# Optimization experiments

Hardware: AMD Instinct MI355X
Metric: run time of the kernel (lower is better)

## Reference

```python
import jax, jax.numpy as jnp
import numpy as np

N_NODES = 20000
IN_DIM = 128      # in_dim(125) + 3
HIDDEN = 256
HEADS = 3
OUT_DIM = 384
NEG_SLOPE = 0.2


def _glorot(key, shape):
    fan_in, fan_out = shape[0], shape[-1]
    lim = (6.0 / (fan_in + fan_out)) ** 0.5
    return jax.random.uniform(key, shape, jnp.float32, -lim, lim)


def setup_inputs() -> dict:
    key = jax.random.key(0)
    ks = jax.random.split(key, 12)
    x = jax.random.normal(ks[0], (N_NODES, IN_DIM), jnp.float32)
    edge_index = jax.random.randint(ks[1], (2, 320000), 0, N_NODES, jnp.int64)
    return {
        "x": x,
        "edge_index": edge_index,
        # gat1: IN_DIM -> HEADS*HIDDEN (concat)
        "W1": _glorot(ks[2], (IN_DIM, HEADS * HIDDEN)),
        "att_src1": _glorot(ks[3], (HEADS, HIDDEN)),
        "att_dst1": _glorot(ks[4], (HEADS, HIDDEN)),
        "b1": jnp.zeros((HEADS * HIDDEN,), jnp.float32),
        # gat2: HEADS*HIDDEN -> OUT_DIM (1 head)
        "W2": _glorot(ks[5], (HEADS * HIDDEN, OUT_DIM)),
        "att_src2": _glorot(ks[6], (1, OUT_DIM)),
        "att_dst2": _glorot(ks[7], (1, OUT_DIM)),
        "b2": jnp.zeros((OUT_DIM,), jnp.float32),
    }


def _gat_layer(x, src, dst, W, a_src, a_dst, bias, heads, out_ch):
    """PyG GATConv: per-head linear, LeakyReLU attention logits,
    segment-softmax over incoming edges (grouped by dst), scatter-add."""
    n = x.shape[0]
    h = (x @ W).reshape(n, heads, out_ch)               # [N,H,C]
    al_s = jnp.einsum('nhc,hc->nh', h, a_src)            # [N,H]
    al_d = jnp.einsum('nhc,hc->nh', h, a_dst)            # [N,H]
    e = jax.nn.leaky_relu(al_s[src] + al_d[dst], NEG_SLOPE)  # [E,H]
    e_max = jax.ops.segment_max(e, dst, num_segments=n)      # [N,H]
    e_exp = jnp.exp(e - e_max[dst])
    denom = jax.ops.segment_sum(e_exp, dst, num_segments=n)  # [N,H]
    alpha = e_exp / denom[dst]                               # [E,H]
    msg = h[src] * alpha[:, :, None]                         # [E,H,C]
    out = jax.ops.segment_sum(msg, dst, num_segments=n)      # [N,H,C]
    return out.reshape(n, heads * out_ch) + bias


def reference(x, edge_index, W1, att_src1, att_dst1, b1, W2, att_src2, att_dst2, b2):
    n = x.shape[0]
    # PyG GATConv default add_self_loops=True
    loops = jnp.arange(n, dtype=edge_index.dtype)
    src = jnp.concatenate([edge_index[0], loops])
    dst = jnp.concatenate([edge_index[1], loops])
    h = _gat_layer(x, src, dst, W1, att_src1, att_dst1, b1, HEADS, HIDDEN)
    h = jax.nn.relu(h)
    h = _gat_layer(h, src, dst, W2, att_src2, att_dst2, b2, 1, OUT_DIM)
    return jax.nn.relu(h)  # mode='node' -> [N, OUT_DIM]
```

## Files before the change

### kernel.cpp

```cpp
#include <hip/hip_runtime.h>
#include <hip/hip_bf16.h>

#define NEG_SLOPE 0.2f

typedef _Float16 half8 __attribute__((ext_vector_type(8)));
typedef _Float16 half4v __attribute__((ext_vector_type(4)));
typedef _Float16 half2v __attribute__((ext_vector_type(2)));
typedef float floatx4 __attribute__((ext_vector_type(4)));
typedef float floatx2 __attribute__((ext_vector_type(2)));

__global__ void k_hist(const int* __restrict__ dst, int E, int n, int* __restrict__ deg) {
    int e = blockIdx.x * blockDim.x + threadIdx.x;
    int ET = E + n;
    if (e >= ET) return;
    int d = (e < E) ? dst[e] : (e - E);
    atomicAdd(&deg[d], 1);
}

__global__ void k_scan1(const int* __restrict__ deg, int* __restrict__ bsum, int n) {
    __shared__ int red[256];
    int t = threadIdx.x, b = blockIdx.x;
    int i = b * 256 + t;
    red[t] = (i < n) ? deg[i] : 0;
    __syncthreads();
    for (int off = 128; off; off >>= 1) {
        if (t < off) red[t] += red[t + off];
        __syncthreads();
    }
    if (t == 0) bsum[b] = red[0];
}

__global__ void k_scan3(const int* __restrict__ deg, const int* __restrict__ bsum,
                        int nb, int* __restrict__ rowptr, int* __restrict__ cursor,
                        int n) {
    __shared__ int s[256];
    int t = threadIdx.x, b = blockIdx.x;
    s[t] = (t < nb) ? bsum[t] : 0;
    __syncthreads();
    for (int off = 1; off < 256; off <<= 1) {
        int v = (t >= off) ? s[t - off] : 0;
        __syncthreads();
        s[t] += v;
        __syncthreads();
    }
    int base = (b == 0) ? 0 : s[b - 1];
    __syncthreads();
    int i = b * 256 + t;
    int v = (i < n) ? deg[i] : 0;
    s[t] = v;
    __syncthreads();
    for (int off = 1; off < 256; off <<= 1) {
        int u = (t >= off) ? s[t - off] : 0;
        __syncthreads();
        s[t] += u;
        __syncthreads();
    }
    int incl = s[t];
    if (i < n) {
        rowptr[i] = base + incl - v;
        cursor[i] = base + incl - v;
        if (i == n - 1) rowptr[n] = base + incl;
    }
}

__global__ void k_scatter(const int* __restrict__ src, const int* __restrict__ dst,
                          int E, int n, int* __restrict__ cursor,
                          int* __restrict__ csr_src) {
    int e = blockIdx.x * blockDim.x + threadIdx.x;
    int ET = E + n;
    if (e >= ET) return;
    int s = (e < E) ? src[e] : (e - E);
    int d = (e < E) ? dst[e] : (e - E);
    int pos = atomicAdd(&cursor[d], 1);
    csr_src[pos] = s;
}

__global__ void k_wprep(const float* __restrict__ W1, const float* __restrict__ W2,
                        const float* __restrict__ as1, const float* __restrict__ ad1,
                        const float* __restrict__ as2, const float* __restrict__ ad2,
                        _Float16* __restrict__ w1t, _Float16* __restrict__ w2t,
                        float* __restrict__ vs1, float* __restrict__ vd1,
                        float* __restrict__ vs2, float* __restrict__ vd2) {
    int b = blockIdx.x;
    if (b < 384) {
        int i = b * 256 + threadIdx.x;
        int c = i / 128, r = i % 128;
        w1t[i] = (_Float16)W1[(size_t)r * 768 + c];
    } else if (b < 1536) {
        int i = (b - 384) * 256 + threadIdx.x;
        int c = i / 768, r = i % 768;
        w2t[i] = (_Float16)W2[(size_t)r * 384 + c];
    } else if (b < 1538) {
        int t = (b - 1536) * 256 + threadIdx.x;
        if (t < 384) {
            int h = t >> 7, k = t & 127;
            const float* wr = W1 + (size_t)k * 768 + h * 256;
            const float* ar = as1 + h * 256;
            const float* dr = ad1 + h * 256;
            float s = 0.f, d = 0.f;
            for (int c = 0; c < 256; ++c) { float wv = wr[c]; s += wv * ar[c]; d += wv * dr[c]; }
            vs1[t] = s; vd1[t] = d;
        }
    } else {
        int t = (b - 1538) * 256 + threadIdx.x;
        if (t < 768) {
            const float* wr = W2 + (size_t)t * 384;
            float s = 0.f, d = 0.f;
            for (int c = 0; c < 384; ++c) { float wv = wr[c]; s += wv * as2[c]; d += wv * ad2[c]; }
            vs2[t] = s; vd2[t] = d;
        }
    }
}

__global__ __launch_bounds__(256) void k_prep1(const float* __restrict__ x,
        _Float16* __restrict__ xh, const float* __restrict__ vs,
        const float* __restrict__ vd, float* __restrict__ al_s,
        float* __restrict__ al_d, int n) {
    int wid = (blockIdx.x * blockDim.x + threadIdx.x) >> 6;
    int lane = threadIdx.x & 63;
    if (wid >= n) return;
    float2 f = *(const float2*)(x + (size_t)wid * 128 + lane * 2);
    half2v hv; hv[0] = (_Float16)f.x; hv[1] = (_Float16)f.y;
    *(half2v*)(xh + (size_t)wid * 128 + lane * 2) = hv;
    float aS[3], aD[3];
#pragma unroll
    for (int hh = 0; hh < 3; ++hh) {
        floatx2 v = *(const floatx2*)(vs + hh * 128 + lane * 2);
        floatx2 d = *(const floatx2*)(vd + hh * 128 + lane * 2);
        aS[hh] = f.x * v[0] + f.y * v[1];
        aD[hh] = f.x * d[0] + f.y * d[1];
    }
#pragma unroll
    for (int hh = 0; hh < 3; ++hh)
#pragma unroll
        for (int off = 32; off; off >>= 1) {
            aS[hh] += __shfl_xor(aS[hh], off);
            aD[hh] += __shfl_xor(aD[hh], off);
        }
    if (lane == 0) {
#pragma unroll
        for (int hh = 0; hh < 3; ++hh) { al_s[wid * 3 + hh] = aS[hh]; al_d[wid * 3 + hh] = aD[hh]; }
    }
}

__global__ __launch_bounds__(256) void k_aggx(const _Float16* __restrict__ xh,
                                              const float* __restrict__ al_s,
                                              const float* __restrict__ al_d,
                                              const int* __restrict__ rowptr,
                                              const int* __restrict__ csr_src,
                                              _Float16* __restrict__ xagg,
                                              int n) {
    int wid = (blockIdx.x * blockDim.x + threadIdx.x) >> 6;
    int lane = threadIdx.x & 63;
    if (wid >= n) return;
    int beg = rowptr[wid], end = rowptr[wid + 1];
    int slot = lane >> 4;
    int chunk = lane & 15;

    float ald0 = al_d[wid * 3 + 0], ald1 = al_d[wid * 3 + 1], ald2 = al_d[wid * 3 + 2];

    float acc0[8] = {}, acc1[8] = {}, acc2[8] = {};
    float sw0 = 0.f, sw1 = 0.f, sw2 = 0.f;

    for (int base = beg; base < end; base += 8) {
        int eA = base + slot, eB = base + 4 + slot;
        bool vA = eA < end, vB = eB < end;
        int sA = vA ? csr_src[eA] : 0;
        int sB = vB ? csr_src[eB] : 0;
        float wA0 = 0.f, wA1 = 0.f, wA2 = 0.f, wB0 = 0.f, wB1 = 0.f, wB2 = 0.f;
        if (vA) {
            float e0 = al_s[sA * 3 + 0] + ald0; e0 = e0 > 0.f ? e0 : NEG_SLOPE * e0;
            float e1 = al_s[sA * 3 + 1] + ald1; e1 = e1 > 0.f ? e1 : NEG_SLOPE * e1;
            float e2 = al_s[sA * 3 + 2] + ald2; e2 = e2 > 0.f ? e2 : NEG_SLOPE * e2;
            wA0 = __expf(e0); wA1 = __expf(e1); wA2 = __expf(e2);
        }
        if (vB) {
            float e0 = al_s[sB * 3 + 0] + ald0; e0 = e0 > 0.f ? e0 : NEG_SLOPE * e0;
            float e1 = al_s[sB * 3 + 1] + ald1; e1 = e1 > 0.f ? e1 : NEG_SLOPE * e1;
            float e2 = al_s[sB * 3 + 2] + ald2; e2 = e2 > 0.f ? e2 : NEG_SLOPE * e2;
            wB0 = __expf(e0); wB1 = __expf(e1); wB2 = __expf(e2);
        }
        sw0 += wA0 + wB0; sw1 += wA1 + wB1; sw2 += wA2 + wB2;
        half8 xvA = *(const half8*)(xh + (size_t)sA * 128 + chunk * 8);
        half8 xvB = *(const half8*)(xh + (size_t)sB * 128 + chunk * 8);
#pragma unroll
        for (int k = 0; k < 8; ++k) {
            float fA = (float)xvA[k], fB = (float)xvB[k];
            acc0[k] = fmaf(wA0, fA, acc0[k]); acc0[k] = fmaf(wB0, fB, acc0[k]);
            acc1[k] = fmaf(wA1, fA, acc1[k]); acc1[k] = fmaf(wB1, fB, acc1[k]);
            acc2[k] = fmaf(wA2, fA, acc2[k]); acc2[k] = fmaf(wB2, fB, acc2[k]);
        }
    }
#pragma unroll
    for (int k = 0; k < 8; ++k) {
        acc0[k] += __shfl_xor(acc0[k], 16); acc0[k] += __shfl_xor(acc0[k], 32);
        acc1[k] += __shfl_xor(acc1[k], 16); acc1[k] += __shfl_xor(acc1[k], 32);
        acc2[k] += __shfl_xor(acc2[k], 16); acc2[k] += __shfl_xor(acc2[k], 32);
    }
    sw0 += __shfl_xor(sw0, 16); sw0 += __shfl_xor(sw0, 32);
    sw1 += __shfl_xor(sw1, 16); sw1 += __shfl_xor(sw1, 32);
    sw2 += __shfl_xor(sw2, 16); sw2 += __shfl_xor(sw2, 32);

    if (lane < 16) {
        float i0 = 1.f / sw0, i1 = 1.f / sw1, i2 = 1.f / sw2;
        _Float16* op = xagg + (size_t)wid * 384 + chunk * 8;
        half8 o0, o1, o2;
#pragma unroll
        for (int k = 0; k < 8; ++k) {
            o0[k] = (_Float16)(acc0[k] * i0);
            o1[k] = (_Float16)(acc1[k] * i1);
            o2[k] = (_Float16)(acc2[k] * i2);
        }
        *(half8*)(op + 0)   = o0;
        *(half8*)(op + 128) = o1;
        *(half8*)(op + 256) = o2;
    }
}

__device__ __forceinline__ void gload_lds16(const _Float16* g, _Float16* l) {
    __builtin_amdgcn_global_load_lds((const __attribute__((address_space(1))) void*)g,
                                     (__attribute__((address_space(3))) void*)l,
                                     16, 0, 0);
}

template <typename OutT, bool GAT>
__global__ __launch_bounds__(256) void k_hgemm(const _Float16* __restrict__ A,
                                               const _Float16* __restrict__ Bt,
                                               const float* __restrict__ bias,
                                               const float* __restrict__ vs2,
                                               const float* __restrict__ vd2,
                                               float* __restrict__ alS2,
                                               float* __restrict__ alD2,
                                               OutT* __restrict__ C,
                                               int M, int N, int K) {
    __shared__ _Float16 lds[2 * 8192];
    int t = threadIdx.x;
    int lane = t & 63, w = t >> 6;
    int wr = w >> 1, wc = w & 1;
    int lrow = lane & 15, lko = lane >> 4;
    int row0 = blockIdx.y * 128, col0 = blockIdx.x * 128;

    int sr = t & 127;
    int sko = t >> 7;
    int agr = row0 + sr; if (agr >= M) agr = M - 1;
    const _Float16* aRow;
    if constexpr (GAT) {
        int head = col0 >> 8;
        aRow = A + (size_t)agr * 384 + head * 128;
    } else {
        aRow = A + (size_t)agr * K;
    }
    const _Float16* bRow = Bt + (size_t)(col0 + sr) * K;

    floatx4 acc[4][4] = {};

    int nk = K >> 5;
#pragma unroll
    for (int s = 0; s < 2; ++s) {
        int ko = s * 2 + sko;
        gload_lds16(aRow + ko * 8, lds + s * 2048 + t * 8);
        gload_lds16(bRow + ko * 8, lds + 4096 + s * 2048 + t * 8);
    }
    __syncthreads();

    for (int ks = 0; ks < nk; ++ks) {
        int buf = ks & 1;
        if (ks + 1 < nk) {
            int kt = (ks + 1) << 5;
            _Float16* dstb = lds + (buf ^ 1) * 8192;
#pragma unroll
            for (int s = 0; s < 2; ++s) {
                int ko = s * 2 + sko;
                gload_lds16(aRow + kt + ko * 8, dstb + s * 2048 + t * 8);
                gload_lds16(bRow + kt + ko * 8, dstb + 4096 + s * 2048 + t * 8);
            }
        }
        const _Float16* base = lds + buf * 8192 + lko * 1024;
        half8 af[4], bf[4];
#pragma unroll
        for (int mi = 0; mi < 4; ++mi)
            af[mi] = *(const half8*)(base + (wr * 64 + mi * 16 + lrow) * 8);
#pragma unroll
        for (int ni = 0; ni < 4; ++ni)
            bf[ni] = *(const half8*)(base + 4096 + (wc * 64 + ni * 16 + lrow) * 8);
#pragma unroll
        for (int mi = 0; mi < 4; ++mi)
#pragma unroll
            for (int ni = 0; ni < 4; ++ni)
                acc[mi][ni] = __builtin_amdgcn_mfma_f32_16x16x32_f16(
                    af[mi], bf[ni], acc[mi][ni], 0, 0, 0);
        __syncthreads();
    }

#pragma unroll
    for (int mi = 0; mi < 4; ++mi) {
#pragma unroll
        for (int j = 0; j < 4; ++j) {
            int row = row0 + wr * 64 + mi * 16 + lko * 4 + j;
            float ps = 0.f, pd = 0.f;
#pragma unroll
            for (int ni = 0; ni < 4; ++ni) {
                int col = col0 + wc * 64 + ni * 16 + lrow;
                float v = acc[mi][ni][j];
                if constexpr (GAT) {
                    v += bias[col]; v = v > 0.f ? v : 0.f;
                    ps = fmaf(v, vs2[col], ps);
                    pd = fmaf(v, vd2[col], pd);
                }
                if (row < M) C[(size_t)row * N + col] = (OutT)v;
            }
            if constexpr (GAT) {
                if (row >= M) { ps = 0.f; pd = 0.f; }
#pragma unroll
                for (int off = 1; off < 16; off <<= 1) {
                    ps += __shfl_xor(ps, off);
                    pd += __shfl_xor(pd, off);
                }
                if (lrow == 0 && row < M) {
                    atomicAdd(&alS2[row], ps);
                    atomicAdd(&alD2[row], pd);
                }
            }
        }
    }
}

__global__ __launch_bounds__(256) void k_aggw2(const _Float16* __restrict__ h,
                                               const float* __restrict__ al_s,
                                               const float* __restrict__ al_d,
                                               const int* __restrict__ rowptr,
                                               const int* __restrict__ csr_src,
                                               const float* __restrict__ bias,
                                               float* __restrict__ out, int n) {
    constexpr int HC = 384;
    constexpr int CA = 4;
    constexpr int CB = 2;
    int wv = threadIdx.x >> 6;
    int lane = threadIdx.x & 63;
    int node = blockIdx.x * 2 + (wv >> 1);
    int half = wv & 1;
    int ns = wv >> 1;

    __shared__ float s_acc[2][64][CA + CB];
    __shared__ float s_sw[2];

    int beg = rowptr[node], end = rowptr[node + 1];
    float ald = al_d[node];

    float accA[CA] = {}, accB[CB] = {};
    float swsum = 0.f;

    for (int base = beg + half; base < end; base += 128) {
        int myi = base + 2 * lane;
        bool valid = myi < end;
        int sl = valid ? csr_src[myi] : 0;
        float wl = 0.f;
        if (valid) {
            float e = al_s[sl] + ald;
            e = e > 0.f ? e : NEG_SLOPE * e;
            wl = __expf(e);
        }
        swsum += wl;
        int cnt = min(64, (end - base + 1) >> 1);
        int j = 0;
        for (; j + 4 <= cnt; j += 4) {
            int ss0 = __shfl(sl, j + 0), ss1 = __shfl(sl, j + 1);
            int ss2 = __shfl(sl, j + 2), ss3 = __shfl(sl, j + 3);
            float wA0 = __shfl(wl, j + 0), wA1 = __shfl(wl, j + 1);
            float wA2 = __shfl(wl, j + 2), wA3 = __shfl(wl, j + 3);
            const _Float16* r0 = h + (size_t)ss0 * HC;
            const _Float16* r1 = h + (size_t)ss1 * HC;
            const _Float16* r2 = h + (size_t)ss2 * HC;
            const _Float16* r3 = h + (size_t)ss3 * HC;
            half4v va0 = *(const half4v*)(r0 + lane * 4);
            half4v va1 = *(const half4v*)(r1 + lane * 4);
            half4v va2 = *(const half4v*)(r2 + lane * 4);
            half4v va3 = *(const half4v*)(r3 + lane * 4);
            half2v vb0 = *(const half2v*)(r0 + 256 + lane * 2);
            half2v vb1 = *(const half2v*)(r1 + 256 + lane * 2);
            half2v vb2 = *(const half2v*)(r2 + 256 + lane * 2);
            half2v vb3 = *(const half2v*)(r3 + 256 + lane * 2);
#pragma unroll
            for (int k = 0; k < 4; ++k) {
                accA[k] = fmaf(wA0, (float)va0[k], accA[k]);
                accA[k] = fmaf(wA1, (float)va1[k], accA[k]);
                accA[k] = fmaf(wA2, (float)va2[k], accA[k]);
                accA[k] = fmaf(wA3, (float)va3[k], accA[k]);
            }
#pragma unroll
            for (int k = 0; k < 2; ++k) {
                accB[k] = fmaf(wA0, (float)vb0[k], accB[k]);
                accB[k] = fmaf(wA1, (float)vb1[k], accB[k]);
                accB[k] = fmaf(wA2, (float)vb2[k], accB[k]);
                accB[k] = fmaf(wA3, (float)vb3[k], accB[k]);
            }
        }
        for (; j < cnt; ++j) {
            int s = __shfl(sl, j);
            float aA = __shfl(wl, j);
            const _Float16* row = h + (size_t)s * HC;
            half4v va = *(const half4v*)(row + lane * 4);
            half2v vb = *(const half2v*)(row + 256 + lane * 2);
#pragma unroll
            for (int k = 0; k < 4; ++k) accA[k] = fmaf(aA, (float)va[k], accA[k]);
#pragma unroll
            for (int k = 0; k < 2; ++k) accB[k] = fmaf(aA, (float)vb[k], accB[k]);
        }
    }

#pragma unroll
    for (int off = 32; off; off >>= 1) swsum += __shfl_xor(swsum, off);

    if (half == 1) {
#pragma unroll
        for (int k = 0; k < CA; ++k) s_acc[ns][lane][k] = accA[k];
#pragma unroll
        for (int k = 0; k < CB; ++k) s_acc[ns][lane][CA + k] = accB[k];
        if (lane == 0) s_sw[ns] = swsum;
    }
    __syncthreads();
    if (half == 1) return;

#pragma unroll
    for (int k = 0; k < CA; ++k) accA[k] += s_acc[ns][lane][k];
#pragma unroll
    for (int k = 0; k < CB; ++k) accB[k] += s_acc[ns][lane][CA + k];
    float inv = 1.f / (swsum + s_sw[ns]);

    size_t obase = (size_t)node * HC;
    int cA0 = lane * CA, cB0 = 64 * CA + lane * CB;
    float4 oa;
    float t0 = accA[0] * inv + bias[cA0 + 0]; oa.x = t0 > 0.f ? t0 : 0.f;
    float t1 = accA[1] * inv + bias[cA0 + 1]; oa.y = t1 > 0.f ? t1 : 0.f;
    float t2 = accA[2] * inv + bias[cA0 + 2]; oa.z = t2 > 0.f ? t2 : 0.f;
    float t3 = accA[3] * inv + bias[cA0 + 3]; oa.w = t3 > 0.f ? t3 : 0.f;
    *(float4*)(out + obase + cA0) = oa;
    floatx2 ob;
    float u0 = accB[0] * inv + bias[cB0 + 0]; ob[0] = u0 > 0.f ? u0 : 0.f;
    float u1 = accB[1] * inv + bias[cB0 + 1]; ob[1] = u1 > 0.f ? u1 : 0.f;
    *(floatx2*)(out + obase + cB0) = ob;
}

extern "C" void kernel_launch(void* const* d_in, const int* in_sizes, int n_in,
                              void* d_out, int out_size, void* d_ws, size_t ws_size,
                              hipStream_t stream) {
    const float* x   = (const float*)d_in[0];
    const int*   ei  = (const int*)d_in[1];
    const float* W1  = (const float*)d_in[2];
    const float* as1 = (const float*)d_in[3];
    const float* ad1 = (const float*)d_in[4];
    const float* b1  = (const float*)d_in[5];
    const float* W2  = (const float*)d_in[6];
    const float* as2 = (const float*)d_in[7];
    const float* ad2 = (const float*)d_in[8];
    const float* b2  = (const float*)d_in[9];
    float* out = (float*)d_out;

    const int N  = in_sizes[0] / 128;
    const int E  = in_sizes[1] / 2;
    const int ET = E + N;
    const int NB = (N + 255) / 256;
    const int* src = ei;
    const int* dst = ei + E;

    char* ws = (char*)d_ws;
    size_t off = 0;
    auto alloc = [&](size_t bytes) {
        void* p = ws + off;
        off = (off + bytes + 255) & ~(size_t)255;
        return p;
    };
    _Float16* xh    = (_Float16*)alloc((size_t)N * 128 * 2);
    _Float16* xagg  = (_Float16*)alloc((size_t)N * 384 * 2);
    _Float16* x2h   = (_Float16*)alloc((size_t)N * 768 * 2);
    _Float16* h2    = (_Float16*)alloc((size_t)N * 384 * 2);
    _Float16* w1t   = (_Float16*)alloc((size_t)768 * 128 * 2);
    _Float16* w2t   = (_Float16*)alloc((size_t)384 * 768 * 2);
    float* vs1  = (float*)alloc(384 * 4);
    float* vd1  = (float*)alloc(384 * 4);
    float* vs2  = (float*)alloc(768 * 4);
    float* vd2  = (float*)alloc(768 * 4);
    float* alS1 = (float*)alloc((size_t)N * 3 * 4);
    float* alD1 = (float*)alloc((size_t)N * 3 * 4);
    int*   deg  = (int*)alloc((size_t)N * 4);
    float* alS2 = (float*)alloc((size_t)N * 4);
    float* alD2 = (float*)alloc((size_t)N * 4);
    int* rowptr = (int*)alloc((size_t)(N + 1) * 4);
    int* cursor = (int*)alloc((size_t)N * 4);
    int* bsum   = (int*)alloc(256 * 4);
    int* csrs   = (int*)alloc((size_t)ET * 4);

    hipMemsetAsync(deg, 0, (size_t)((char*)rowptr - (char*)deg), stream);

    k_hist<<<(ET + 255) / 256, 256, 0, stream>>>(dst, E, N, deg);
    k_scan1<<<NB, 256, 0, stream>>>(deg, bsum, N);
    k_scan3<<<NB, 256, 0, stream>>>(deg, bsum, NB, rowptr, cursor, N);
    k_scatter<<<(ET + 255) / 256, 256, 0, stream>>>(src, dst, E, N, cursor, csrs);

    k_wprep<<<1541, 256, 0, stream>>>(W1, W2, as1, ad1, as2, ad2,
                                      w1t, w2t, vs1, vd1, vs2, vd2);

    k_prep1<<<(N + 3) / 4, 256, 0, stream>>>(x, xh, vs1, vd1, alS1, alD1, N);
    k_aggx<<<(N + 3) / 4, 256, 0, stream>>>(xh, alS1, alD1, rowptr, csrs, xagg, N);
    dim3 g1(768 / 128, (N + 127) / 128);
    k_hgemm<_Float16, true><<<g1, 256, 0, stream>>>(xagg, w1t, b1, vs2, vd2,
                                                    alS2, alD2, x2h, N, 768, 128);

    dim3 g2(384 / 128, (N + 127) / 128);
    k_hgemm<_Float16, false><<<g2, 256, 0, stream>>>(x2h, w2t, nullptr, nullptr,
                                                     nullptr, nullptr, nullptr,
                                                     h2, N, 384, 768);
    k_aggw2<<<N / 2, 256, 0, stream>>>(h2, alS2, alD2, rowptr, csrs, b2, out, N);
}
```

Measured before the change: 211.3 us.

## Split layer-2 features into three 128-column tables for gather locality

The second GEMM now writes its 384-wide fp16 output as three separate N×128 column-slab tables instead of row-major rows. The final aggregation kernel gathers each slab in a separate pass over the neighbor list, so every lane reads a contiguous 256-byte slice per neighbor row. The idea is a smaller per-pass gather working set and better cache hit rates. In exchange, the shuffles and index math are repeated three times, and the GEMM epilogue stores are more scattered.

```diff
diff --git a/kernel.cpp b/kernel.cpp
--- a/kernel.cpp
+++ b/kernel.cpp
@@ -292,6 +292,7 @@
         __syncthreads();
     }
 
+    size_t tblstride = (size_t)M * 128;
 #pragma unroll
     for (int mi = 0; mi < 4; ++mi) {
 #pragma unroll
@@ -306,8 +307,11 @@
                     v += bias[col]; v = v > 0.f ? v : 0.f;
                     ps = fmaf(v, vs2[col], ps);
                     pd = fmaf(v, vd2[col], pd);
+                    if (row < M) C[(size_t)row * N + col] = (OutT)v;
+                } else {
+                    if (row < M)
+                        C[(size_t)(col >> 7) * tblstride + (size_t)row * 128 + (col & 127)] = (OutT)v;
                 }
-                if (row < M) C[(size_t)row * N + col] = (OutT)v;
             }
             if constexpr (GAT) {
                 if (row >= M) { ps = 0.f; pd = 0.f; }
@@ -325,29 +329,27 @@
     }
 }
 
-__global__ __launch_bounds__(256) void k_aggw2(const _Float16* __restrict__ h,
+__global__ __launch_bounds__(256) void k_aggw2(const _Float16* __restrict__ h2s,
                                                const float* __restrict__ al_s,
                                                const float* __restrict__ al_d,
                                                const int* __restrict__ rowptr,
                                                const int* __restrict__ csr_src,
                                                const float* __restrict__ bias,
                                                float* __restrict__ out, int n) {
-    constexpr int HC = 384;
-    constexpr int CA = 4;
-    constexpr int CB = 2;
     int wv = threadIdx.x >> 6;
     int lane = threadIdx.x & 63;
     int node = blockIdx.x * 2 + (wv >> 1);
     int half = wv & 1;
     int ns = wv >> 1;
 
-    __shared__ float s_acc[2][64][CA + CB];
+    __shared__ float s_acc[2][64][6];
     __shared__ float s_sw[2];
 
     int beg = rowptr[node], end = rowptr[node + 1];
     float ald = al_d[node];
-
-    float accA[CA] = {}, accB[CB] = {};
+    size_t tbl = (size_t)n * 128;
+
+    float acc[3][2] = {};
     float swsum = 0.f;
 
     for (int base = beg + half; base < end; base += 128) {
@@ -362,50 +364,36 @@
         }
         swsum += wl;
         int cnt = min(64, (end - base + 1) >> 1);
-        int j = 0;
-        for (; j + 4 <= cnt; j += 4) {
-            int ss0 = __shfl(sl, j + 0), ss1 = __shfl(sl, j + 1);
-            int ss2 = __shfl(sl, j + 2), ss3 = __shfl(sl, j + 3);
-            float wA0 = __shfl(wl, j + 0), wA1 = __shfl(wl, j + 1);
-            float wA2 = __shfl(wl, j + 2), wA3 = __shfl(wl, j + 3);
-            const _Float16* r0 = h + (size_t)ss0 * HC;
-            const _Float16* r1 = h + (size_t)ss1 * HC;
-            const _Float16* r2 = h + (size_t)ss2 * HC;
-            const _Float16* r3 = h + (size_t)ss3 * HC;
-            half4v va0 = *(const half4v*)(r0 + lane * 4);
-            half4v va1 = *(const half4v*)(r1 + lane * 4);
-            half4v va2 = *(const half4v*)(r2 + lane * 4);
-            half4v va3 = *(const half4v*)(r3 + lane * 4);
-            half2v vb0 = *(const half2v*)(r0 + 256 + lane * 2);
-            half2v vb1 = *(const half2v*)(r1 + 256 + lane * 2);
-            half2v vb2 = *(const half2v*)(r2 + 256 + lane * 2);
-            half2v vb3 = *(const half2v*)(r3 + 256 + lane * 2);
-#pragma unroll
-            for (int k = 0; k < 4; ++k) {
-                accA[k] = fmaf(wA0, (float)va0[k], accA[k]);
-                accA[k] = fmaf(wA1, (float)va1[k], accA[k]);
-                accA[k] = fmaf(wA2, (float)va2[k], accA[k]);
-                accA[k] = fmaf(wA3, (float)va3[k], accA[k]);
+#pragma unroll
+        for (int t = 0; t < 3; ++t) {
+            const _Float16* T = h2s + (size_t)t * tbl;
+            int j = 0;
+            for (; j + 4 <= cnt; j += 4) {
+                int ss0 = __shfl(sl, j + 0), ss1 = __shfl(sl, j + 1);
+                int ss2 = __shfl(sl, j + 2), ss3 = __shfl(sl, j + 3);
+                float w0 = __shfl(wl, j + 0), w1 = __shfl(wl, j + 1);
+                float w2 = __shfl(wl, j + 2), w3 = __shfl(wl, j + 3);
+                half2v v0 = *(const half2v*)(T + (size_t)ss0 * 128 + lane * 2);
+                half2v v1 = *(const half2v*)(T + (size_t)ss1 * 128 + lane * 2);
+                half2v v2 = *(const half2v*)(T + (size_t)ss2 * 128 + lane * 2);
+                half2v v3 = *(const half2v*)(T + (size_t)ss3 * 128 + lane * 2);
+                acc[t][0] = fmaf(w0, (float)v0[0], acc[t][0]);
+                acc[t][1] = fmaf(w0, (float)v0[1], acc[t][1]);
+                acc[t][0] = fmaf(w1, (float)v1[0], acc[t][0]);
+                acc[t][1] = fmaf(w1, (float)v1[1], acc[t][1]);
+                acc[t][0] = fmaf(w2, (float)v2[0], acc[t][0]);
+                acc[t][1] = fmaf(w2, (float)v2[1], acc[t][1]);
+                acc[t][0] = fmaf(w3, (float)v3[0], acc[t][0]);
+                acc[t][1] = fmaf(w3, (float)v3[1], acc[t][1]);
             }
-#pragma unroll
-            for (int k = 0; k < 2; ++k) {
-                accB[k] = fmaf(wA0, (float)vb0[k], accB[k]);
-                accB[k] = fmaf(wA1, (float)vb1[k], accB[k]);
-                accB[k] = fmaf(wA2, (float)vb2[k], accB[k]);
-                accB[k] = fmaf(wA3, (float)vb3[k], accB[k]);
+            for (; j < cnt; ++j) {
+                int s = __shfl(sl, j);
+                float ww = __shfl(wl, j);
+                half2v v = *(const half2v*)(T + (size_t)s * 128 + lane * 2);
+                acc[t][0] = fmaf(ww, (float)v[0], acc[t][0]);
+                acc[t][1] = fmaf(ww, (float)v[1], acc[t][1]);
             }
         }
-        for (; j < cnt; ++j) {
-            int s = __shfl(sl, j);
-            float aA = __shfl(wl, j);
-            const _Float16* row = h + (size_t)s * HC;
-            half4v va = *(const half4v*)(row + lane * 4);
-            half2v vb = *(const half2v*)(row + 256 + lane * 2);
-#pragma unroll
-            for (int k = 0; k < 4; ++k) accA[k] = fmaf(aA, (float)va[k], accA[k]);
-#pragma unroll
-            for (int k = 0; k < 2; ++k) accB[k] = fmaf(aA, (float)vb[k], accB[k]);
-        }
     }
 
 #pragma unroll
@@ -413,32 +401,27 @@
 
     if (half == 1) {
 #pragma unroll
-        for (int k = 0; k < CA; ++k) s_acc[ns][lane][k] = accA[k];
-#pragma unroll
-        for (int k = 0; k < CB; ++k) s_acc[ns][lane][CA + k] = accB[k];
+        for (int t = 0; t < 3; ++t) {
+            s_acc[ns][lane][t * 2 + 0] = acc[t][0];
+            s_acc[ns][lane][t * 2 + 1] = acc[t][1];
+        }
         if (lane == 0) s_sw[ns] = swsum;
     }
     __syncthreads();
     if (half == 1) return;
 
-#pragma unroll
-    for (int k = 0; k < CA; ++k) accA[k] += s_acc[ns][lane][k];
-#pragma unroll
-    for (int k = 0; k < CB; ++k) accB[k] += s_acc[ns][lane][CA + k];
     float inv = 1.f / (swsum + s_sw[ns]);
-
-    size_t obase = (size_t)node * HC;
-    int cA0 = lane * CA, cB0 = 64 * CA + lane * CB;
-    float4 oa;
-    float t0 = accA[0] * inv + bias[cA0 + 0]; oa.x = t0 > 0.f ? t0 : 0.f;
-    float t1 = accA[1] * inv + bias[cA0 + 1]; oa.y = t1 > 0.f ? t1 : 0.f;
-    float t2 = accA[2] * inv + bias[cA0 + 2]; oa.z = t2 > 0.f ? t2 : 0.f;
-    float t3 = accA[3] * inv + bias[cA0 + 3]; oa.w = t3 > 0.f ? t3 : 0.f;
-    *(float4*)(out + obase + cA0) = oa;
-    floatx2 ob;
-    float u0 = accB[0] * inv + bias[cB0 + 0]; ob[0] = u0 > 0.f ? u0 : 0.f;
-    float u1 = accB[1] * inv + bias[cB0 + 1]; ob[1] = u1 > 0.f ? u1 : 0.f;
-    *(floatx2*)(out + obase + cB0) = ob;
+    size_t obase = (size_t)node * 384;
+#pragma unroll
+    for (int t = 0; t < 3; ++t) {
+        int ch = t * 128 + lane * 2;
+        float a0 = (acc[t][0] + s_acc[ns][lane][t * 2 + 0]) * inv + bias[ch];
+        float a1 = (acc[t][1] + s_acc[ns][lane][t * 2 + 1]) * inv + bias[ch + 1];
+        floatx2 o;
+        o[0] = a0 > 0.f ? a0 : 0.f;
+        o[1] = a1 > 0.f ? a1 : 0.f;
+        *(floatx2*)(out + obase + ch) = o;
+    }
 }
 
 extern "C" void kernel_launch(void* const* d_in, const int* in_sizes, int n_in,
@@ -473,7 +456,7 @@
     _Float16* xh    = (_Float16*)alloc((size_t)N * 128 * 2);
     _Float16* xagg  = (_Float16*)alloc((size_t)N * 384 * 2);
     _Float16* x2h   = (_Float16*)alloc((size_t)N * 768 * 2);
-    _Float16* h2    = (_Float16*)alloc((size_t)N * 384 * 2);
+    _Float16* h2s   = (_Float16*)alloc((size_t)N * 384 * 2);
     _Float16* w1t   = (_Float16*)alloc((size_t)768 * 128 * 2);
     _Float16* w2t   = (_Float16*)alloc((size_t)384 * 768 * 2);
     float* vs1  = (float*)alloc(384 * 4);
@@ -509,6 +492,6 @@
     dim3 g2(384 / 128, (N + 127) / 128);
     k_hgemm<_Float16, false><<<g2, 256, 0, stream>>>(x2h, w2t, nullptr, nullptr,
                                                      nullptr, nullptr, nullptr,
-                                                     h2, N, 384, 768);
-    k_aggw2<<<N / 2, 256, 0, stream>>>(h2, alS2, alD2, rowptr, csrs, b2, out, N);
-}
+                                                     h2s, N, 384, 768);
+    k_aggw2<<<N / 2, 256, 0, stream>>>(h2s, alS2, alD2, rowptr, csrs, b2, out, N);
+}
```

New measurement: 214.6 us. No clear change (+1.5%).
